# Kernel optimization log

Hardware: AMD Instinct MI355X
Metric: run time of the kernel (lower is better)

## Reference

```python
import jax, jax.numpy as jnp
import numpy as np

CUTOFF = 5.0
EPS = 1e-7
N = 50000
L = 160.0


def _cart3(a, b, c):
    # cartesian product of ranges [-a..a] x [-b..b] x [-c..c], row-major like torch.cartesian_prod
    A, B, C = np.meshgrid(np.arange(-a, a + 1), np.arange(-b, b + 1), np.arange(-c, c + 1), indexing='ij')
    return np.stack([A.ravel(), B.ravel(), C.ravel()], axis=1)


def wrap_positions(positions, cell):
    scaled = positions @ jnp.linalg.inv(cell) + EPS
    scaled = scaled % 1.0 - EPS
    return scaled @ cell


def setup_inputs() -> dict:
    key = jax.random.key(0)
    positions = jax.random.uniform(key, (N, 3), dtype=jnp.float32) * L
    cell = jnp.eye(3, dtype=jnp.float32) * L
    return {"positions": positions, "cell": cell}


def reference(positions, cell):
    wrapped = wrap_positions(positions, cell)

    cell_np = np.asarray(cell, dtype=np.float64)
    norm_a = np.linalg.norm(np.cross(cell_np[1], cell_np[2]))
    norm_b = np.linalg.norm(np.cross(cell_np[2], cell_np[0]))
    norm_c = np.linalg.norm(np.cross(cell_np[0], cell_np[1]))
    volume = float(np.dot(cell_np[0], np.cross(cell_np[1], cell_np[2])))
    pa = int(np.ceil(CUTOFF * norm_a / volume))
    pb = int(np.ceil(CUTOFF * norm_b / volume))
    pc = int(np.ceil(CUTOFF * norm_c / volume))

    pad_mat = jnp.asarray(_cart3(pa, pb, pc), dtype=positions.dtype)  # [P,3]
    P = pad_mat.shape[0]
    n = wrapped.shape[0]

    # replicate atoms into all periodic images: index k -> atom k//P, image k%P
    padded_pos = (wrapped[:, None, :] + pad_mat @ cell).reshape(-1, 3)  # [n*P,3]
    padded_cpos = jnp.floor(padded_pos / CUTOFF).astype(jnp.int32)
    corner = padded_cpos.min(axis=0)
    padded_cpos = padded_cpos - corner
    shap = np.asarray(padded_cpos.max(axis=0)) + 1
    num_cells = int(shap.prod())
    count_vec = jnp.asarray([int(shap[1] * shap[2]), int(shap[2]), 1], dtype=jnp.int32)

    padded_cind = (padded_cpos * count_vec).sum(axis=1)  # linear cell id per padded atom
    padded_gind = jnp.arange(n * P, dtype=jnp.int32) + 1  # 1-based so 0 == empty slot
    padded_rind = jnp.repeat(jnp.arange(n, dtype=jnp.int32), P)  # real-atom id of each image

    atom_cpos = jnp.floor(wrapped / CUTOFF).astype(jnp.int32) - corner
    disp = jnp.asarray(_cart3(1, 1, 1), dtype=jnp.int32)  # 27-cell stencil
    atom_cnind = ((atom_cpos[:, None, :] + disp) * count_vec).sum(axis=-1)  # [n,27]

    # stable sort by cell id, then within-cell rank (== torch unique_consecutive bookkeeping)
    cind_np = np.asarray(padded_cind)
    order = np.argsort(cind_np, kind='stable')
    sorted_cind = cind_np[order]
    _, counts = np.unique(sorted_cind, return_counts=True)
    max_anum = int(counts.max())
    starts = np.repeat(np.cumsum(counts) - counts, counts)
    ranks = np.arange(sorted_cind.shape[0]) - starts

    gci = jnp.zeros((num_cells, max_anum, 2), dtype=jnp.int32)
    gci = gci.at[sorted_cind, ranks, 0].set(padded_gind[order])
    gci = gci.at[sorted_cind, ranks, 1].set(padded_rind[order])

    atom_nind = gci[atom_cnind]  # [n,27,max_anum,2]
    occ = np.asarray(atom_nind[..., 0])
    pair_i, neigh, jslot = np.nonzero(occ)
    pair_jp = occ[pair_i, neigh, jslot] - 1  # index into padded_pos
    pair_j = np.asarray(atom_nind[..., 1])[pair_i, neigh, jslot]

    pair_diff = padded_pos[pair_jp] - wrapped[pair_i]
    pair_dist = jnp.linalg.norm(pair_diff, axis=1)
    mask = np.asarray((pair_dist < CUTOFF) & (pair_dist > 0.01))
    keep = np.nonzero(mask)[0]

    pairs = jnp.stack([jnp.asarray(pair_i, jnp.int32), jnp.asarray(pair_j, jnp.int32)], axis=1)
    return pairs[keep], pair_diff[keep], pair_dist[keep]
```

## Files before the change

kernel.cpp:

```cpp
#include <hip/hip_runtime.h>


#define CUTOFF 5.0f
#define WEPS   1e-7f
#define PIMG   27
#define G      36
#define NCELLS (G*G*G)
#define SLOT   16
#define NT1    256
#define NB2    2048
#define NT2    256
#define JPT    3
#define CAP    16
#define CSTR   17
#define BCAP   512
#define IMAX   0x7FFFFFFF
#define PRUNE2 25.001f


__device__ __forceinline__ void inv_diag3(const float* __restrict__ cell, float inv[9]) {
  float c[9];
#pragma unroll
  for (int i = 0; i < 9; i++) c[i] = cell[i];
  float a00=c[0],a01=c[1],a02=c[2],a10=c[3],a11=c[4],a12=c[5],a20=c[6],a21=c[7],a22=c[8];
  float m00 = __fsub_rn(__fmul_rn(a11,a22), __fmul_rn(a12,a21));
  float m01 = __fsub_rn(__fmul_rn(a10,a22), __fmul_rn(a12,a20));
  float m02 = __fsub_rn(__fmul_rn(a10,a21), __fmul_rn(a11,a20));
  float det = __fadd_rn(__fsub_rn(__fmul_rn(a00,m00), __fmul_rn(a01,m01)), __fmul_rn(a02,m02));
  inv[0] = __fdiv_rn(m00, det);
  inv[1] = __fdiv_rn(__fsub_rn(__fmul_rn(a02,a21), __fmul_rn(a01,a22)), det);
  inv[2] = __fdiv_rn(__fsub_rn(__fmul_rn(a01,a12), __fmul_rn(a02,a11)), det);
  inv[3] = __fdiv_rn(__fsub_rn(__fmul_rn(a12,a20), __fmul_rn(a10,a22)), det);
  inv[4] = __fdiv_rn(__fsub_rn(__fmul_rn(a00,a22), __fmul_rn(a02,a20)), det);
  inv[5] = __fdiv_rn(__fsub_rn(__fmul_rn(a02,a10), __fmul_rn(a00,a12)), det);
  inv[6] = __fdiv_rn(m02, det);
  inv[7] = __fdiv_rn(__fsub_rn(__fmul_rn(a01,a20), __fmul_rn(a00,a21)), det);
  inv[8] = __fdiv_rn(__fsub_rn(__fmul_rn(a00,a11), __fmul_rn(a01,a10)), det);
}

__device__ __forceinline__ int axis_opts(float w, float cdiag, int* pcomp, int* cellv,
                                         float* shv) {
  int cc = (int)floorf(__fdiv_rn(w, CUTOFF));
  int k = 0;
  if (cc >= 29) {
    float wp = __fsub_rn(w, cdiag);
    int c2 = (int)floorf(__fdiv_rn(wp, CUTOFF)) + 2;
    if ((unsigned)c2 < G) { pcomp[k] = 0; cellv[k] = c2; shv[k] = __fsub_rn(0.0f, cdiag); k++; }
  }
  pcomp[k] = 1; cellv[k] = cc + 2; shv[k] = 0.0f; k++;
  if (cc <= 2) {
    float wp = __fadd_rn(w, cdiag);
    int c2 = (int)floorf(__fdiv_rn(wp, CUTOFF)) + 2;
    if ((unsigned)c2 < G) { pcomp[k] = 2; cellv[k] = c2; shv[k] = cdiag; k++; }
  }
  return k;
}

__device__ __forceinline__ bool dist_ok(float4 f, float4 w) {
  float ax = __fsub_rn(f.x, w.x), ay = __fsub_rn(f.y, w.y), az = __fsub_rn(f.z, w.z);
  float d = __fsqrt_rn(__fadd_rn(__fadd_rn(__fmul_rn(ax, ax), __fmul_rn(ay, ay)),
                                 __fmul_rn(az, az)));
  return (d < CUTOFF && d > 0.01f);
}

__device__ __forceinline__ unsigned match_mask(const float4* __restrict__ cdata,
                                               int base, int cnt, float4 w) {
  unsigned mask = 0;
  for (int q = 0; q < cnt; q++)
    if (dist_ok(cdata[base + q], w)) mask |= 1u << q;
  return mask;
}

__device__ __forceinline__ int pick_min_t(const float4* __restrict__ cdata, int base,
                                          unsigned mask) {
  int bq = -1, bt = IMAX;
  for (unsigned m2 = mask; m2; m2 &= m2 - 1) {
    int q = __builtin_ctz(m2);
    int t = __float_as_int(cdata[base + q].w);
    if (t < bt) { bt = t; bq = q; }
  }
  return bq;
}

__device__ __forceinline__ float axis_q(float w, int c) {
  float lo = (float)((c - 2) * 5);
  float t = w - lo;
  float v = fmaxf(fmaxf(-t, t - 5.0f), 0.0f);
  return v * v;
}

__device__ __forceinline__ void cswap(int& a, int& b) {
  int lo = min(a, b), hi = max(a, b);
  a = lo; b = hi;
}

__device__ __forceinline__ int exscan256(int v, int* lds, int* total) {
  int tid = threadIdx.x, lane = tid & 63, wave = tid >> 6;
  int x = v;
#pragma unroll
  for (int off = 1; off < 64; off <<= 1) {
    int y = __shfl_up(x, off);
    if (lane >= off) x += y;
  }
  if (lane == 63) lds[wave] = x;
  __syncthreads();
  if (wave == 0) {
    int wv = (lane < 4) ? lds[lane] : 0;
#pragma unroll
    for (int off = 1; off < 4; off <<= 1) {
      int y = __shfl_up(wv, off);
      if (lane >= off) wv += y;
    }
    if (lane < 4) lds[lane] = wv;
  }
  __syncthreads();
  int wbase = (wave == 0) ? 0 : lds[wave - 1];
  *total = lds[3];
  __syncthreads();
  return wbase + x - v;
}

__device__ __forceinline__ int exscan1024(int v, int* lds, int* total) {
  int tid = threadIdx.x, lane = tid & 63, wave = tid >> 6;
  int x = v;
#pragma unroll
  for (int off = 1; off < 64; off <<= 1) {
    int y = __shfl_up(x, off);
    if (lane >= off) x += y;
  }
  if (lane == 63) lds[wave] = x;
  __syncthreads();
  if (wave == 0) {
    int wv = (lane < 16) ? lds[lane] : 0;
#pragma unroll
    for (int off = 1; off < 16; off <<= 1) {
      int y = __shfl_up(wv, off);
      if (lane >= off) wv += y;
    }
    if (lane < 16) lds[lane] = wv;
  }
  __syncthreads();
  int wbase = (wave == 0) ? 0 : lds[wave - 1];
  *total = lds[15];
  __syncthreads();
  return wbase + x - v;
}

__global__ void __launch_bounds__(NT1)
k_build(const float* __restrict__ pos, const float* __restrict__ cell,
        int* __restrict__ fill, float4* __restrict__ wrapped,
        float4* __restrict__ cdata, int n) {
  const int ai = blockIdx.x * NT1 + threadIdx.x;
  if (ai >= n) return;
  float inv[9];
  inv_diag3(cell, inv);
  float px = pos[3*ai], py = pos[3*ai+1], pz = pos[3*ai+2];
  float m[3];
#pragma unroll
  for (int col = 0; col < 3; col++) {
    float s = __fadd_rn(__fadd_rn(__fmul_rn(px, inv[col]), __fmul_rn(py, inv[3+col])),
                        __fmul_rn(pz, inv[6+col]));
    s = __fadd_rn(s, WEPS);
    float t = __fsub_rn(s, floorf(s));
    m[col] = __fsub_rn(t, WEPS);
  }
  float wx = __fadd_rn(__fadd_rn(__fmul_rn(m[0], cell[0]), __fmul_rn(m[1], cell[3])),
                       __fmul_rn(m[2], cell[6]));
  float wy = __fadd_rn(__fadd_rn(__fmul_rn(m[0], cell[1]), __fmul_rn(m[1], cell[4])),
                       __fmul_rn(m[2], cell[7]));
  float wz = __fadd_rn(__fadd_rn(__fmul_rn(m[0], cell[2]), __fmul_rn(m[1], cell[5])),
                       __fmul_rn(m[2], cell[8]));
  wrapped[ai] = make_float4(wx, wy, wz, 0.0f);
  int px_[2], py_[2], pz_[2], cx_[2], cy_[2], cz_[2];
  float sx_[2], sy_[2], sz_[2];
  int nx = axis_opts(wx, cell[0], px_, cx_, sx_);
  int ny = axis_opts(wy, cell[4], py_, cy_, sy_);
  int nz = axis_opts(wz, cell[8], pz_, cz_, sz_);
  for (int a = 0; a < nx; a++)
    for (int b = 0; b < ny; b++)
      for (int c = 0; c < nz; c++) {
        int cid = (cx_[a] * G + cy_[b]) * G + cz_[c];
        int p = (px_[a] * 3 + py_[b]) * 3 + pz_[c];
        int slot = atomicAdd(&fill[cid], 1);
        if (slot < SLOT)
          cdata[cid * SLOT + slot] =
              make_float4(__fadd_rn(wx, sx_[a]), __fadd_rn(wy, sy_[b]),
                          __fadd_rn(wz, sz_[c]), __int_as_float(ai * PIMG + p));
      }
}

__global__ void __launch_bounds__(NT2)
k_pair(const float4* __restrict__ wrapped, const int* __restrict__ fill,
       const float4* __restrict__ cdata, int2* __restrict__ paddr,
       int* __restrict__ blockSum, int n) {
  __shared__ int lds[8];
  __shared__ int pcache[NT2 * CSTR];
  const int tid = threadIdx.x, blk = blockIdx.x;
  const int n27 = n * PIMG;
  const int tbase = (blk * NT2 + tid) * JPT;
  const int i0 = min(tbase, n27 - 1) / PIMG;
  const int i1 = min(tbase + JPT - 1, n27 - 1) / PIMG;
  const float4 w0 = wrapped[i0];
  const float4 w1 = wrapped[i1];
  const int cx0 = (int)floorf(__fdiv_rn(w0.x, CUTOFF)) + 2;
  const int cy0 = (int)floorf(__fdiv_rn(w0.y, CUTOFF)) + 2;
  const int cz0 = (int)floorf(__fdiv_rn(w0.z, CUTOFF)) + 2;
  const int cx1 = (int)floorf(__fdiv_rn(w1.x, CUTOFF)) + 2;
  const int cy1 = (int)floorf(__fdiv_rn(w1.y, CUTOFF)) + 2;
  const int cz1 = (int)floorf(__fdiv_rn(w1.z, CUTOFF)) + 2;
  int bases[JPT], cnts[JPT];
#pragma unroll
  for (int j = 0; j < JPT; j++) {
    int idx = tbase + j;
    bool valid = idx < n27;
    int ic = valid ? idx / PIMG : i0;
    int s27 = valid ? idx - ic * PIMG : 0;
    bool a0 = (ic == i0);
    int ix = s27 / 9, iy = (s27 / 3) % 3, iz = s27 % 3;
    float wxs = a0 ? w0.x : w1.x, wys = a0 ? w0.y : w1.y, wzs = a0 ? w0.z : w1.z;
    int cx = (a0 ? cx0 : cx1) + ix - 1;
    int cy = (a0 ? cy0 : cy1) + iy - 1;
    int cz = (a0 ? cz0 : cz1) + iz - 1;
    float ps = axis_q(wxs, cx) + axis_q(wys, cy) + axis_q(wzs, cz);
    bool keep = valid && (ps <= PRUNE2);
    int cid = (cx * G + cy) * G + cz;
    bases[j] = cid * SLOT;
    cnts[j] = keep ? min(fill[cid], SLOT) : 0;
  }
  int tcnt = 0, c0 = 0;
#pragma unroll
  for (int j = 0; j < JPT; j++) {
    bool a0 = (tbase + j) < (i0 + 1) * PIMG;
    float4 w = a0 ? w0 : w1;
    int base = bases[j], cnt = cnts[j];
    if (cnt > 0) {
      if (cnt <= 4) {
        float4 f0 = cdata[base + 0];
        float4 f1 = cdata[base + 1];
        float4 f2 = cdata[base + 2];
        float4 f3 = cdata[base + 3];
        int a = (cnt > 0 && dist_ok(f0, w)) ? (__float_as_int(f0.w) * 16 + 0) : IMAX;
        int b = (cnt > 1 && dist_ok(f1, w)) ? (__float_as_int(f1.w) * 16 + 1) : IMAX;
        int c = (cnt > 2 && dist_ok(f2, w)) ? (__float_as_int(f2.w) * 16 + 2) : IMAX;
        int d = (cnt > 3 && dist_ok(f3, w)) ? (__float_as_int(f3.w) * 16 + 3) : IMAX;
        cswap(a, b); cswap(c, d); cswap(a, c); cswap(b, d); cswap(b, c);
        if (a != IMAX) { if (tcnt < CAP) pcache[tid * CSTR + tcnt] = base + (a & 15); tcnt++; }
        if (b != IMAX) { if (tcnt < CAP) pcache[tid * CSTR + tcnt] = base + (b & 15); tcnt++; }
        if (c != IMAX) { if (tcnt < CAP) pcache[tid * CSTR + tcnt] = base + (c & 15); tcnt++; }
        if (d != IMAX) { if (tcnt < CAP) pcache[tid * CSTR + tcnt] = base + (d & 15); tcnt++; }
      } else {
        unsigned mask = match_mask(cdata, base, cnt, w);
        while (mask) {
          int bq = pick_min_t(cdata, base, mask);
          mask &= ~(1u << bq);
          if (tcnt < CAP) pcache[tid * CSTR + tcnt] = base + bq;
          tcnt++;
        }
      }
    }
    if (a0) c0 = tcnt;
  }
  int btotal;
  const int texcl = exscan256(tcnt, lds, &btotal);
  if (tid == 0) blockSum[blk] = btotal;
  int2* dst = paddr + (size_t)blk * BCAP;
  if (tcnt <= CAP) {
    for (int k = 0; k < tcnt; k++) {
      int o = texcl + k;
      if (o < BCAP) dst[o] = make_int2(pcache[tid * CSTR + k], (k < c0) ? i0 : i1);
    }
  } else {
    int o = texcl;
#pragma unroll
    for (int j = 0; j < JPT; j++) {
      bool a0 = (tbase + j) < (i0 + 1) * PIMG;
      float4 w = a0 ? w0 : w1;
      int i = a0 ? i0 : i1;
      int base = bases[j];
      unsigned mask = match_mask(cdata, base, cnts[j], w);
      while (mask) {
        int bq = pick_min_t(cdata, base, mask);
        mask &= ~(1u << bq);
        if (o < BCAP) dst[o] = make_int2(base + bq, i);
        o++;
      }
    }
  }
}

__global__ void __launch_bounds__(1024)
k_scan(const int* __restrict__ blockSum, int* __restrict__ blockBase,
       float* __restrict__ out, int K) {
  __shared__ int lds[32];
  const int tid = threadIdx.x;
  int s0 = blockSum[2 * tid], s1 = blockSum[2 * tid + 1];
  int total;
  int ex = exscan1024(s0 + s1, lds, &total);
  blockBase[2 * tid] = ex;
  blockBase[2 * tid + 1] = ex + s0;
  if (tid == 0 && total != K) {
    float code = (total < K) ? (1000000.0f + (float)min(K - total, 100000))
                             : (2000000.0f + (float)min(total - K, 100000));
    for (int t = 0; t < 256; t++) out[t] = code;
  }
}

__global__ void __launch_bounds__(NT2)
k_emit(const float4* __restrict__ wrapped, const float4* __restrict__ cdata,
       const int2* __restrict__ paddr, const int* __restrict__ blockSum,
       const int* __restrict__ blockBase, float* __restrict__ out, int K) {
  const int blk = blockIdx.x;
  const int bs = min(blockSum[blk], BCAP);
  const int base = blockBase[blk];
  const int2* src = paddr + (size_t)blk * BCAP;
  for (int l = threadIdx.x; l < bs; l += NT2) {
    int2 e = src[l];
    float4 f = cdata[e.x];
    float4 w = wrapped[e.y];
    int o = base + l;
    float ax = __fsub_rn(f.x, w.x), ay = __fsub_rn(f.y, w.y), az = __fsub_rn(f.z, w.z);
    float d = __fsqrt_rn(__fadd_rn(__fadd_rn(__fmul_rn(ax, ax), __fmul_rn(ay, ay)),
                                   __fmul_rn(az, az)));
    if (o >= 0 && o < K) {
      int tt = __float_as_int(f.w);
      ((float2*)out)[o] = make_float2((float)e.y, (float)(tt / PIMG));
      size_t db = (size_t)2 * K + (size_t)3 * o;
      out[db]     = ax;
      out[db + 1] = ay;
      out[db + 2] = az;
      out[(size_t)5 * K + o] = d;
    }
  }
}

extern "C" void kernel_launch(void* const* d_in, const int* in_sizes, int n_in,
                              void* d_out, int out_size, void* d_ws, size_t ws_size,
                              hipStream_t stream) {
  const float* pos  = (const float*)d_in[0];
  const float* cell = (const float*)d_in[1];
  float* out = (float*)d_out;
  int n = in_sizes[0] / 3;
  int K = out_size / 6;

  char* ws = (char*)d_ws;
  size_t off = 0;
  auto alloc = [&](size_t bytes) -> char* {
    char* p = ws + off;
    off = (off + bytes + 255) & ~(size_t)255;
    return p;
  };
  int*    fill      = (int*)alloc((size_t)NCELLS * 4);
  size_t  zbytes    = off;
  float4* wrapped   = (float4*)alloc((size_t)n * 16);
  float4* cdata     = (float4*)alloc((size_t)NCELLS * SLOT * 16);
  int2*   paddr     = (int2*)alloc((size_t)NB2 * BCAP * 8);
  int*    blockSum  = (int*)alloc((size_t)NB2 * 4);
  int*    blockBase = (int*)alloc((size_t)NB2 * 4);
  if (off > ws_size) return;

  (void)hipMemsetAsync(fill, 0, zbytes, stream);
  int nb1 = (n + NT1 - 1) / NT1;
  k_build<<<nb1, NT1, 0, stream>>>(pos, cell, fill, wrapped, cdata, n);
  k_pair<<<NB2, NT2, 0, stream>>>(wrapped, fill, cdata, paddr, blockSum, n);
  k_scan<<<1, 1024, 0, stream>>>(blockSum, blockBase, out, K);
  k_emit<<<NB2, NT2, 0, stream>>>(wrapped, cdata, paddr, blockSum, blockBase, out, K);
}
```

Baseline: 98.63 us.

## Fold scan into emit kernel and skip loads of empty cell slots

The single-block scan kernel is removed. Each emit block now computes its own output offset by summing the blockSum entries of all earlier blocks with a block reduction, and block 0 also checks the grand total against K. This drops one kernel launch and the serial dependency on it, at the cost of redundant reads of up to 2048 counts per block. In the pair kernel, the slot loads for small cells are now conditional on the cell count, so unused slots are no longer read.

```diff
diff --git a/kernel.cpp b/kernel.cpp
--- a/kernel.cpp
+++ b/kernel.cpp
@@ -116,32 +116,6 @@
   __syncthreads();
   int wbase = (wave == 0) ? 0 : lds[wave - 1];
   *total = lds[3];
-  __syncthreads();
-  return wbase + x - v;
-}
-
-__device__ __forceinline__ int exscan1024(int v, int* lds, int* total) {
-  int tid = threadIdx.x, lane = tid & 63, wave = tid >> 6;
-  int x = v;
-#pragma unroll
-  for (int off = 1; off < 64; off <<= 1) {
-    int y = __shfl_up(x, off);
-    if (lane >= off) x += y;
-  }
-  if (lane == 63) lds[wave] = x;
-  __syncthreads();
-  if (wave == 0) {
-    int wv = (lane < 16) ? lds[lane] : 0;
-#pragma unroll
-    for (int off = 1; off < 16; off <<= 1) {
-      int y = __shfl_up(wv, off);
-      if (lane >= off) wv += y;
-    }
-    if (lane < 16) lds[lane] = wv;
-  }
-  __syncthreads();
-  int wbase = (wave == 0) ? 0 : lds[wave - 1];
-  *total = lds[15];
   __syncthreads();
   return wbase + x - v;
 }
@@ -236,9 +210,14 @@
     if (cnt > 0) {
       if (cnt <= 4) {
         float4 f0 = cdata[base + 0];
-        float4 f1 = cdata[base + 1];
-        float4 f2 = cdata[base + 2];
-        float4 f3 = cdata[base + 3];
+        float4 f1 = f0, f2 = f0, f3 = f0;
+        if (cnt > 1) {
+          f1 = cdata[base + 1];
+          if (cnt > 2) {
+            f2 = cdata[base + 2];
+            if (cnt > 3) f3 = cdata[base + 3];
+          }
+        }
         int a = (cnt > 0 && dist_ok(f0, w)) ? (__float_as_int(f0.w) * 16 + 0) : IMAX;
         int b = (cnt > 1 && dist_ok(f1, w)) ? (__float_as_int(f1.w) * 16 + 1) : IMAX;
         int c = (cnt > 2 && dist_ok(f2, w)) ? (__float_as_int(f2.w) * 16 + 2) : IMAX;
@@ -288,32 +267,42 @@
   }
 }
 
-__global__ void __launch_bounds__(1024)
-k_scan(const int* __restrict__ blockSum, int* __restrict__ blockBase,
-       float* __restrict__ out, int K) {
-  __shared__ int lds[32];
-  const int tid = threadIdx.x;
-  int s0 = blockSum[2 * tid], s1 = blockSum[2 * tid + 1];
-  int total;
-  int ex = exscan1024(s0 + s1, lds, &total);
-  blockBase[2 * tid] = ex;
-  blockBase[2 * tid + 1] = ex + s0;
-  if (tid == 0 && total != K) {
-    float code = (total < K) ? (1000000.0f + (float)min(K - total, 100000))
-                             : (2000000.0f + (float)min(total - K, 100000));
-    for (int t = 0; t < 256; t++) out[t] = code;
-  }
-}
-
 __global__ void __launch_bounds__(NT2)
 k_emit(const float4* __restrict__ wrapped, const float4* __restrict__ cdata,
        const int2* __restrict__ paddr, const int* __restrict__ blockSum,
-       const int* __restrict__ blockBase, float* __restrict__ out, int K) {
-  const int blk = blockIdx.x;
+       float* __restrict__ out, int K) {
+  __shared__ int lds[8];
+  const int tid = threadIdx.x, blk = blockIdx.x;
+  const int lane = tid & 63, wave = tid >> 6;
+  int partial = 0;
+  for (int idx = tid; idx < blk; idx += NT2) partial += blockSum[idx];
+  int v = partial;
+#pragma unroll
+  for (int off = 32; off; off >>= 1) v += __shfl_xor(v, off);
+  if (lane == 0) lds[wave] = v;
+  __syncthreads();
+  const int base = lds[0] + lds[1] + lds[2] + lds[3];
+  if (blk == 0) {
+    __syncthreads();
+    int p2 = 0;
+    for (int idx = tid; idx < NB2; idx += NT2) p2 += blockSum[idx];
+    int v2 = p2;
+#pragma unroll
+    for (int off = 32; off; off >>= 1) v2 += __shfl_xor(v2, off);
+    if (lane == 0) lds[wave] = v2;
+    __syncthreads();
+    if (tid == 0) {
+      int total = lds[0] + lds[1] + lds[2] + lds[3];
+      if (total != K) {
+        float code = (total < K) ? (1000000.0f + (float)min(K - total, 100000))
+                                 : (2000000.0f + (float)min(total - K, 100000));
+        for (int t = 0; t < 256; t++) out[t] = code;
+      }
+    }
+  }
   const int bs = min(blockSum[blk], BCAP);
-  const int base = blockBase[blk];
   const int2* src = paddr + (size_t)blk * BCAP;
-  for (int l = threadIdx.x; l < bs; l += NT2) {
+  for (int l = tid; l < bs; l += NT2) {
     int2 e = src[l];
     float4 f = cdata[e.x];
     float4 w = wrapped[e.y];
@@ -349,19 +338,17 @@
     off = (off + bytes + 255) & ~(size_t)255;
     return p;
   };
-  int*    fill      = (int*)alloc((size_t)NCELLS * 4);
-  size_t  zbytes    = off;
-  float4* wrapped   = (float4*)alloc((size_t)n * 16);
-  float4* cdata     = (float4*)alloc((size_t)NCELLS * SLOT * 16);
-  int2*   paddr     = (int2*)alloc((size_t)NB2 * BCAP * 8);
-  int*    blockSum  = (int*)alloc((size_t)NB2 * 4);
-  int*    blockBase = (int*)alloc((size_t)NB2 * 4);
+  int*    fill     = (int*)alloc((size_t)NCELLS * 4);
+  size_t  zbytes   = off;
+  float4* wrapped  = (float4*)alloc((size_t)n * 16);
+  float4* cdata    = (float4*)alloc((size_t)NCELLS * SLOT * 16);
+  int2*   paddr    = (int2*)alloc((size_t)NB2 * BCAP * 8);
+  int*    blockSum = (int*)alloc((size_t)NB2 * 4);
   if (off > ws_size) return;
 
   (void)hipMemsetAsync(fill, 0, zbytes, stream);
   int nb1 = (n + NT1 - 1) / NT1;
   k_build<<<nb1, NT1, 0, stream>>>(pos, cell, fill, wrapped, cdata, n);
   k_pair<<<NB2, NT2, 0, stream>>>(wrapped, fill, cdata, paddr, blockSum, n);
-  k_scan<<<1, 1024, 0, stream>>>(blockSum, blockBase, out, K);
-  k_emit<<<NB2, NT2, 0, stream>>>(wrapped, cdata, paddr, blockSum, blockBase, out, K);
-}
+  k_emit<<<NB2, NT2, 0, stream>>>(wrapped, cdata, paddr, blockSum, out, K);
+}
```

New measurement: 101.7 us. 3.1% more time.
